# Kernel tuning notes

Hardware: AMD Instinct MI355X
Metric: run time of the kernel (lower is better)

Reference implementation:

```python
import jax, jax.numpy as jnp
import numpy as np

SCALE_FACTOR = 4.0
DROPOUT_P = 0.5
DROPOUT_KEY = jax.random.key(42)  # fixed key: torch dropout is stochastic; we fix RNG for reproducibility


def setup_inputs() -> dict:
    key = jax.random.key(0)
    k1, k2 = jax.random.split(key)
    x1 = jax.random.normal(k1, (4096, 1024), dtype=jnp.float32)
    x2 = jax.random.normal(k2, (4096, 1024), dtype=jnp.float32)
    return {"x1": x1, "x2": x2}


def reference(x1, x2):
    # scores: [M, N] = x1 @ x2^T, scaled
    scores = jnp.matmul(x1, x2.T) * SCALE_FACTOR
    # F.softmax with no dim on 2-D input -> softmax over dim 1 (keys)
    attn = jax.nn.softmax(scores, axis=-1)
    # dropout p=0.5, train mode (inverted dropout: scale kept units by 1/(1-p))
    keep = jax.random.bernoulli(DROPOUT_KEY, 1.0 - DROPOUT_P, attn.shape)
    attn = jnp.where(keep, attn / (1.0 - DROPOUT_P), 0.0).astype(attn.dtype)
    # output: [M, D] = attn @ x2 (x2 reused as values)
    return jnp.matmul(attn, x2)
```

## Files before the change

kernel.cpp:

```cpp
#include <hip/hip_runtime.h>

typedef unsigned short u16;
typedef unsigned int   u32;
typedef __attribute__((ext_vector_type(4))) float f32x4;
typedef __attribute__((ext_vector_type(8))) short bf16x8;
typedef __attribute__((ext_vector_type(8))) unsigned short u16x8;
typedef __attribute__((ext_vector_type(4))) unsigned short u16x4;

#define MROWS 4096
#define DDIM  1024

__device__ __forceinline__ u16 f2bf(float f) {
  u32 u = __float_as_uint(f);
  return (u16)((u + 0x7FFFu + ((u >> 16) & 1u)) >> 16);
}
__device__ __forceinline__ float bf2f(u16 h) { return __uint_as_float(((u32)h) << 16); }

__device__ __forceinline__ u32 rotl32(u32 x, int r) { return (x << r) | (x >> (32 - r)); }
__device__ __forceinline__ u32 threefry_bits(u32 n) {
  const u32 K0 = 0u, K1 = 42u, K2 = 0x1BD11BDAu ^ 0u ^ 42u;
  u32 x0 = K0;
  u32 x1 = n + K1;
#define TF4(a,b,c,d) \
  x0 += x1; x1 = rotl32(x1, a); x1 ^= x0; \
  x0 += x1; x1 = rotl32(x1, b); x1 ^= x0; \
  x0 += x1; x1 = rotl32(x1, c); x1 ^= x0; \
  x0 += x1; x1 = rotl32(x1, d); x1 ^= x0;
  TF4(13,15,26,6);  x0 += K1; x1 += K2 + 1u;
  TF4(17,29,16,24); x0 += K2; x1 += K0 + 2u;
  TF4(13,15,26,6);  x0 += K0; x1 += K1 + 3u;
  TF4(17,29,16,24); x0 += K1; x1 += K2 + 4u;
  TF4(13,15,26,6);  x0 += K2; x1 += K0 + 5u;
#undef TF4
  return x0 ^ x1;
}

__global__ __launch_bounds__(256)
void expand3(const float4* __restrict__ x, u16* __restrict__ out, float scale, int patA,
             u32* __restrict__ mask, u32 wordBase, u32 nWords) {
  int t = blockIdx.x * 256 + threadIdx.x;
  float4 v0 = x[(size_t)t * 2], v1 = x[(size_t)t * 2 + 1];
  float vv[8] = {v0.x*scale, v0.y*scale, v0.z*scale, v0.w*scale,
                 v1.x*scale, v1.y*scale, v1.z*scale, v1.w*scale};
  u16 o[24];
#pragma unroll
  for (int j = 0; j < 8; ++j) {
    u16 h = f2bf(vv[j]);
    u16 l = f2bf(vv[j] - bf2f(h));
    if (patA) { o[3*j]=h; o[3*j+1]=h; o[3*j+2]=l; }
    else      { o[3*j]=h; o[3*j+1]=l; o[3*j+2]=h; }
  }
  u16x8* dst = (u16x8*)(out + (size_t)t * 24);
#pragma unroll
  for (int q = 0; q < 3; ++q) {
    u16x8 wv;
#pragma unroll
    for (int j = 0; j < 8; ++j) wv[j] = o[q*8+j];
    dst[q] = wv;
  }
  if ((u32)t < nWords) {
    u32 wi = wordBase + (u32)t;
    u32 n0 = wi * 32u;
    u32 wbits = 0;
#pragma unroll 4
    for (int b = 0; b < 32; ++b) wbits |= (threefry_bits(n0 + (u32)b) >> 31) << b;
    mask[wi] = wbits;
  }
}

__global__ __launch_bounds__(256)
void transpose_bf16(const float* __restrict__ x2, u16* __restrict__ VT) {
  __shared__ float tile[64][65];
  int tid = threadIdx.x;
  int dt = blockIdx.x;
  int kt = blockIdx.y;
#pragma unroll
  for (int it = 0; it < 16; ++it) {
    int lin = it * 256 + tid;
    int r = lin >> 6, c = lin & 63;
    tile[r][c] = x2[(size_t)(kt*64 + r) * DDIM + dt*64 + c];
  }
  __syncthreads();
#pragma unroll
  for (int it = 0; it < 16; ++it) {
    int lin = it * 256 + tid;
    int dr = lin >> 6, kc = lin & 63;
    VT[(size_t)(dt*64 + dr) * MROWS + kt*64 + kc] = f2bf(tile[kc][dr]);
  }
}

__device__ __forceinline__ void gload16(const u16* g, u16* l) {
  __builtin_amdgcn_global_load_lds(
      (const __attribute__((address_space(1))) void*)g,
      (__attribute__((address_space(3))) void*)l, 16, 0, 0);
}

#define BARRIER() do { asm volatile("" ::: "memory"); __builtin_amdgcn_s_barrier(); \
                       asm volatile("" ::: "memory"); } while (0)
#define LGKM0()   do { asm volatile("s_waitcnt lgkmcnt(0)" ::: "memory"); \
                       __builtin_amdgcn_sched_barrier(0); } while (0)
#define VMCNT6()  do { asm volatile("s_waitcnt vmcnt(6)" ::: "memory"); } while (0)

__device__ __forceinline__ void mma4x4(f32x4 (&accq)[4][4], const bf16x8 (&a)[4],
                                       const bf16x8 (&b)[4]) {
#pragma unroll
  for (int m = 0; m < 4; ++m)
#pragma unroll
    for (int n = 0; n < 4; ++n)
      accq[m][n] = __builtin_amdgcn_mfma_f32_16x16x32_bf16(a[m], b[n], accq[m][n], 0, 0, 0);
}

__global__ __launch_bounds__(512, 2)
void gemm256(const u16* __restrict__ A, const u16* __restrict__ Bt, float* __restrict__ C,
             int M, int N, int K, int ntpc) {
  __shared__ u16 smem[65536];
  const int tid = threadIdx.x;
  const int lane = tid & 63;
  const int w = tid >> 6;
  const int wr = w >> 2;
  const int wc = w & 3;
  const int fr = lane & 15;
  const int hi = lane >> 4;

  const int nbxy = gridDim.x * gridDim.y;
  const int id0 = blockIdx.y * gridDim.x + blockIdx.x;
  const int id  = (id0 & 7) * (nbxy >> 3) + (id0 >> 3);
  const int bxi = id % gridDim.x;
  const int byi = id / gridDim.x;

  const long bm = (long)byi * 256;
  const long bn = (long)bxi * 256;
  const size_t kcol0 = (size_t)blockIdx.z * ntpc * 64;
  float* Cz = C + (size_t)blockIdx.z * (size_t)M * N;

  const int srow = tid >> 3;
  const int scol = (((tid & 7) ^ (srow & 7)) << 3);
  const u16* Abase = A  + (size_t)(bm + srow) * K + kcol0 + scol;
  const u16* Bbase = Bt + (size_t)(bn + srow) * K + kcol0 + scol;

  const int csw0 = ((hi)     ^ (fr & 7)) << 3;
  const int csw1 = ((4 + hi) ^ (fr & 7)) << 3;
  const int arow = (wr*16 + fr) * 64;
  const int brow = (wc*16 + fr) * 64;

#define RD_A(dst, D, H, CSW) do { \
    const u16* _b = smem + ((D)*2+(H))*8192 + arow + (CSW); \
    dst[0] = *(const bf16x8*)(_b); \
    dst[1] = *(const bf16x8*)(_b + 2048); \
    dst[2] = *(const bf16x8*)(_b + 4096); \
    dst[3] = *(const bf16x8*)(_b + 6144); } while (0)
#define RD_B(dst, D, CSW) do { \
    const u16* _b0 = smem + 32768 + ((D)*2+0)*8192 + brow + (CSW); \
    const u16* _b1 = smem + 32768 + ((D)*2+1)*8192 + brow + (CSW); \
    dst[0] = *(const bf16x8*)(_b0); \
    dst[1] = *(const bf16x8*)(_b0 + 4096); \
    dst[2] = *(const bf16x8*)(_b1); \
    dst[3] = *(const bf16x8*)(_b1 + 4096); } while (0)

  f32x4 accL[4][4], accH[4][4];
#pragma unroll
  for (int m = 0; m < 4; ++m)
#pragma unroll
    for (int n = 0; n < 4; ++n) {
      accL[m][n] = (f32x4){0.f, 0.f, 0.f, 0.f};
      accH[m][n] = (f32x4){0.f, 0.f, 0.f, 0.f};
    }
  bf16x8 aE[4], aO[4], bE[4], bO[4];

#define STAGE_A(TAU,H,D) do { \
    const u16* _s = Abase + (size_t)(H)*128*K + (size_t)(TAU)*64; \
    u16* _d = smem + ((D)*2+(H))*8192 + tid*8; \
    gload16(_s, _d); gload16(_s + (size_t)64*K, _d + 4096); } while (0)
#define STAGE_B(TAU,H,D) do { \
    const u16* _s = Bbase + (size_t)(H)*128*K + (size_t)(TAU)*64; \
    u16* _d = smem + 32768 + ((D)*2+(H))*8192 + tid*8; \
    gload16(_s, _d); gload16(_s + (size_t)64*K, _d + 4096); } while (0)

  STAGE_A(0,0,0); STAGE_B(0,0,0); STAGE_B(0,1,0); STAGE_A(0,1,0);
  STAGE_A(1,0,1); STAGE_B(1,0,1); STAGE_B(1,1,1);
  VMCNT6();
  BARRIER();

  const int nt = ntpc;
  for (int T = 0; T < nt; T += 2) {
    const int t1 = T + 1;
    const int t2 = (T + 2 < nt) ? T + 2 : nt - 1;
    const int t3 = (T + 3 < nt) ? T + 3 : nt - 1;

    RD_A(aE, 0, 0, csw0);
    RD_B(bE, 0, csw0);
    STAGE_A(t1, 1, 1);
    BARRIER(); LGKM0();
    __builtin_amdgcn_s_setprio(1); mma4x4(accL, aE, bE); __builtin_amdgcn_s_setprio(0);
    BARRIER();
    RD_A(aO, 0, 0, csw1);
    RD_B(bO, 0, csw1);
    BARRIER(); LGKM0();
    __builtin_amdgcn_s_setprio(1); mma4x4(accL, aO, bO); __builtin_amdgcn_s_setprio(0);
    BARRIER();
    RD_A(aE, 0, 1, csw0);
    STAGE_A(t2, 0, 0); STAGE_B(t2, 0, 0); STAGE_B(t2, 1, 0);
    BARRIER(); LGKM0();
    __builtin_amdgcn_s_setprio(1); mma4x4(accH, aE, bE); __builtin_amdgcn_s_setprio(0);
    BARRIER();
    RD_A(aO, 0, 1, csw1);
    VMCNT6();
    BARRIER(); LGKM0();
    __builtin_amdgcn_s_setprio(1); mma4x4(accH, aO, bO); __builtin_amdgcn_s_setprio(0);
    BARRIER();
    RD_A(aE, 1, 0, csw0);
    RD_B(bE, 1, csw0);
    STAGE_A(t2, 1, 0);
    BARRIER(); LGKM0();
    __builtin_amdgcn_s_setprio(1); mma4x4(accL, aE, bE); __builtin_amdgcn_s_setprio(0);
    BARRIER();
    RD_A(aO, 1, 0, csw1);
    RD_B(bO, 1, csw1);
    BARRIER(); LGKM0();
    __builtin_amdgcn_s_setprio(1); mma4x4(accL, aO, bO); __builtin_amdgcn_s_setprio(0);
    BARRIER();
    RD_A(aE, 1, 1, csw0);
    STAGE_A(t3, 0, 1); STAGE_B(t3, 0, 1); STAGE_B(t3, 1, 1);
    BARRIER(); LGKM0();
    __builtin_amdgcn_s_setprio(1); mma4x4(accH, aE, bE); __builtin_amdgcn_s_setprio(0);
    BARRIER();
    RD_A(aO, 1, 1, csw1);
    VMCNT6();
    BARRIER(); LGKM0();
    __builtin_amdgcn_s_setprio(1); mma4x4(accH, aO, bO); __builtin_amdgcn_s_setprio(0);
    BARRIER();
  }
#undef STAGE_A
#undef STAGE_B
#undef RD_A
#undef RD_B

#pragma unroll
  for (int m = 0; m < 4; ++m)
#pragma unroll
    for (int n = 0; n < 4; ++n) {
      size_t rowL = (size_t)(bm + m*32 + wr*16 + hi*4);
      size_t rowH = rowL + 128;
      size_t col  = (size_t)(bn + n*64 + wc*16 + fr);
#pragma unroll
      for (int r = 0; r < 4; ++r) {
        Cz[(rowL + r) * N + col] = accL[m][n][r];
        Cz[(rowH + r) * N + col] = accH[m][n][r];
      }
    }
}

__global__ __launch_bounds__(256)
void softmax_dropout(const float* __restrict__ S, const u32* __restrict__ mask,
                     u16* __restrict__ P) {
  const int tid  = threadIdx.x;
  const int lane = tid & 63;
  const int w    = tid >> 6;
  const int row  = blockIdx.x * 4 + w;
  const float4* Sr = (const float4*)(S + (size_t)row * MROWS);
  float4 v[16];
#pragma unroll
  for (int i = 0; i < 16; ++i) v[i] = Sr[i * 64 + lane];
  float m = -3.0e38f;
#pragma unroll
  for (int i = 0; i < 16; ++i)
    m = fmaxf(m, fmaxf(fmaxf(v[i].x, v[i].y), fmaxf(v[i].z, v[i].w)));
#pragma unroll
  for (int off = 32; off > 0; off >>= 1) m = fmaxf(m, __shfl_xor(m, off, 64));
  float s = 0.0f;
#pragma unroll
  for (int i = 0; i < 16; ++i) {
    v[i].x = __expf(v[i].x - m); v[i].y = __expf(v[i].y - m);
    v[i].z = __expf(v[i].z - m); v[i].w = __expf(v[i].w - m);
    s += v[i].x + v[i].y + v[i].z + v[i].w;
  }
#pragma unroll
  for (int off = 32; off > 0; off >>= 1) s += __shfl_xor(s, off, 64);
  const float inv = 2.0f / s;
  u16* Pr = P + (size_t)row * MROWS;
  const u32* Mw = mask + (size_t)row * 128;
#pragma unroll
  for (int i = 0; i < 16; ++i) {
    int j0 = (i * 64 + lane) * 4;
    u32 word = Mw[j0 >> 5];
    int sh = j0 & 31;
    float e[4] = {v[i].x, v[i].y, v[i].z, v[i].w};
    u16x4 o;
#pragma unroll
    for (int c = 0; c < 4; ++c) {
      float val = ((word >> (sh + c)) & 1u) ? 0.0f : e[c] * inv;
      o[c] = f2bf(val);
    }
    *(u16x4*)(Pr + j0) = o;
  }
}

__global__ __launch_bounds__(256)
void reduce4(const float4* __restrict__ p, float4* __restrict__ out) {
  size_t i = (size_t)blockIdx.x * 256 + threadIdx.x;
  const size_t NP = (size_t)MROWS * DDIM / 4;
  float4 a = p[i], b = p[i + NP], c = p[i + 2*NP], d = p[i + 3*NP];
  float4 r;
  r.x = a.x + b.x + c.x + d.x;
  r.y = a.y + b.y + c.y + d.y;
  r.z = a.z + b.z + c.z + d.z;
  r.w = a.w + b.w + c.w + d.w;
  out[i] = r;
}

extern "C" void kernel_launch(void* const* d_in, const int* in_sizes, int n_in,
                              void* d_out, int out_size, void* d_ws, size_t ws_size,
                              hipStream_t stream) {
  const float* x1 = (const float*)d_in[0];
  const float* x2 = (const float*)d_in[1];
  float* out = (float*)d_out;
  char* ws = (char*)d_ws;

  const size_t OFF_XB   = 25165824;
  const size_t OFF_VT   = 50331648;
  const size_t OFF_S    = 58720256;
  const size_t OFF_MASK = 125829120;
  const size_t NEED     = 127926272;
  if (ws_size < NEED) {
    hipMemsetAsync(d_out, 0x7F, (size_t)out_size * sizeof(float), stream);
    return;
  }
  u16*   XA = (u16*)(ws);
  u16*   XB = (u16*)(ws + OFF_XB);
  u16*   VT = (u16*)(ws + OFF_VT);
  float* S  = (float*)(ws + OFF_S);
  float* PT = (float*)(ws + OFF_S);
  u32*   MK = (u32*)(ws + OFF_MASK);
  u16*   P  = (u16*)(ws);

  expand3<<<2048, 256, 0, stream>>>((const float4*)x1, XA, 4.0f, 1, MK, 0u, 262144u);
  expand3<<<2048, 256, 0, stream>>>((const float4*)x2, XB, 1.0f, 0, MK, 262144u, 262144u);
  transpose_bf16<<<dim3(16, 64), 256, 0, stream>>>(x2, VT);
  gemm256<<<dim3(16, 16, 1), 512, 0, stream>>>(XA, XB, S, 4096, 4096, 3072, 48);
  softmax_dropout<<<1024, 256, 0, stream>>>(S, MK, P);
  gemm256<<<dim3(4, 16, 4), 512, 0, stream>>>(P, VT, PT, 4096, 1024, 4096, 16);
  reduce4<<<4096, 256, 0, stream>>>((const float4*)PT, (float4*)out);
}
```

Before: 205.5 us.

## Restructure GEMM pipeline into quadrant MFMAs, bf16 split-K partials, split mask RNG

```diff
diff --git a/kernel.cpp b/kernel.cpp
--- a/kernel.cpp
+++ b/kernel.cpp
@@ -37,7 +37,7 @@
 
 __global__ __launch_bounds__(256)
 void expand3(const float4* __restrict__ x, u16* __restrict__ out, float scale, int patA,
-             u32* __restrict__ mask, u32 wordBase, u32 nWords) {
+             u32* __restrict__ mask, u32 wordBase) {
   int t = blockIdx.x * 256 + threadIdx.x;
   float4 v0 = x[(size_t)t * 2], v1 = x[(size_t)t * 2 + 1];
   float vv[8] = {v0.x*scale, v0.y*scale, v0.z*scale, v0.w*scale,
@@ -58,14 +58,14 @@
     for (int j = 0; j < 8; ++j) wv[j] = o[q*8+j];
     dst[q] = wv;
   }
-  if ((u32)t < nWords) {
-    u32 wi = wordBase + (u32)t;
-    u32 n0 = wi * 32u;
-    u32 wbits = 0;
+  u32 w = wordBase + ((u32)t >> 1);
+  u32 sh = ((u32)t & 1u) << 4;
+  u32 n0 = w * 32u + sh;
+  u32 half = 0;
 #pragma unroll 4
-    for (int b = 0; b < 32; ++b) wbits |= (threefry_bits(n0 + (u32)b) >> 31) << b;
-    mask[wi] = wbits;
-  }
+  for (int b = 0; b < 16; ++b) half |= (threefry_bits(n0 + (u32)b) >> 31) << (sh + b);
+  u32 word = half | (u32)__shfl_xor((int)half, 1, 64);
+  if ((t & 1) == 0) mask[w] = word;
 }
 
 __global__ __launch_bounds__(256)
@@ -97,21 +97,25 @@
 
 #define BARRIER() do { asm volatile("" ::: "memory"); __builtin_amdgcn_s_barrier(); \
                        asm volatile("" ::: "memory"); } while (0)
-#define LGKM0()   do { asm volatile("s_waitcnt lgkmcnt(0)" ::: "memory"); \
-                       __builtin_amdgcn_sched_barrier(0); } while (0)
-#define VMCNT6()  do { asm volatile("s_waitcnt vmcnt(6)" ::: "memory"); } while (0)
-
-__device__ __forceinline__ void mma4x4(f32x4 (&accq)[4][4], const bf16x8 (&a)[4],
-                                       const bf16x8 (&b)[4]) {
-#pragma unroll
-  for (int m = 0; m < 4; ++m)
-#pragma unroll
-    for (int n = 0; n < 4; ++n)
-      accq[m][n] = __builtin_amdgcn_mfma_f32_16x16x32_bf16(a[m], b[n], accq[m][n], 0, 0, 0);
-}
-
+#define VMCNT(N)  asm volatile("s_waitcnt vmcnt(" #N ")" ::: "memory")
+#define PRIO1()   __builtin_amdgcn_s_setprio(1)
+#define PRIO0()   __builtin_amdgcn_s_setprio(0)
+
+__device__ __forceinline__ void mma_quad(f32x4 (&acc)[8][4], const bf16x8 (&aF)[4][2],
+                                         const bf16x8 (&bF)[2][2], int MH, int NH) {
+#pragma unroll
+  for (int kx = 0; kx < 2; ++kx)
+#pragma unroll
+    for (int m = 0; m < 4; ++m)
+#pragma unroll
+      for (int n = 0; n < 2; ++n)
+        acc[MH*4+m][NH*2+n] = __builtin_amdgcn_mfma_f32_16x16x32_bf16(
+            aF[m][kx], bF[n][kx], acc[MH*4+m][NH*2+n], 0, 0, 0);
+}
+
+template <bool OUT16>
 __global__ __launch_bounds__(512, 2)
-void gemm256(const u16* __restrict__ A, const u16* __restrict__ Bt, float* __restrict__ C,
+void gemm256(const u16* __restrict__ A, const u16* __restrict__ Bt, void* __restrict__ Cv,
              int M, int N, int K, int ntpc) {
   __shared__ u16 smem[65536];
   const int tid = threadIdx.x;
@@ -122,16 +126,9 @@
   const int fr = lane & 15;
   const int hi = lane >> 4;
 
-  const int nbxy = gridDim.x * gridDim.y;
-  const int id0 = blockIdx.y * gridDim.x + blockIdx.x;
-  const int id  = (id0 & 7) * (nbxy >> 3) + (id0 >> 3);
-  const int bxi = id % gridDim.x;
-  const int byi = id / gridDim.x;
-
-  const long bm = (long)byi * 256;
-  const long bn = (long)bxi * 256;
+  const long bm = (long)blockIdx.y * 256;
+  const long bn = (long)blockIdx.x * 256;
   const size_t kcol0 = (size_t)blockIdx.z * ntpc * 64;
-  float* Cz = C + (size_t)blockIdx.z * (size_t)M * N;
 
   const int srow = tid >> 3;
   const int scol = (((tid & 7) ^ (srow & 7)) << 3);
@@ -143,29 +140,25 @@
   const int arow = (wr*16 + fr) * 64;
   const int brow = (wc*16 + fr) * 64;
 
-#define RD_A(dst, D, H, CSW) do { \
-    const u16* _b = smem + ((D)*2+(H))*8192 + arow + (CSW); \
-    dst[0] = *(const bf16x8*)(_b); \
-    dst[1] = *(const bf16x8*)(_b + 2048); \
-    dst[2] = *(const bf16x8*)(_b + 4096); \
-    dst[3] = *(const bf16x8*)(_b + 6144); } while (0)
-#define RD_B(dst, D, CSW) do { \
-    const u16* _b0 = smem + 32768 + ((D)*2+0)*8192 + brow + (CSW); \
-    const u16* _b1 = smem + 32768 + ((D)*2+1)*8192 + brow + (CSW); \
-    dst[0] = *(const bf16x8*)(_b0); \
-    dst[1] = *(const bf16x8*)(_b0 + 4096); \
-    dst[2] = *(const bf16x8*)(_b1); \
-    dst[3] = *(const bf16x8*)(_b1 + 4096); } while (0)
-
-  f32x4 accL[4][4], accH[4][4];
-#pragma unroll
-  for (int m = 0; m < 4; ++m)
-#pragma unroll
-    for (int n = 0; n < 4; ++n) {
-      accL[m][n] = (f32x4){0.f, 0.f, 0.f, 0.f};
-      accH[m][n] = (f32x4){0.f, 0.f, 0.f, 0.f};
-    }
-  bf16x8 aE[4], aO[4], bE[4], bO[4];
+#define RD_A(dst, D, H) do { \
+    const u16* _b0 = smem + ((D)*2+(H))*8192 + arow + csw0; \
+    const u16* _b1 = smem + ((D)*2+(H))*8192 + arow + csw1; \
+    dst[0][0] = *(const bf16x8*)(_b0);        dst[0][1] = *(const bf16x8*)(_b1); \
+    dst[1][0] = *(const bf16x8*)(_b0 + 2048); dst[1][1] = *(const bf16x8*)(_b1 + 2048); \
+    dst[2][0] = *(const bf16x8*)(_b0 + 4096); dst[2][1] = *(const bf16x8*)(_b1 + 4096); \
+    dst[3][0] = *(const bf16x8*)(_b0 + 6144); dst[3][1] = *(const bf16x8*)(_b1 + 6144); } while (0)
+#define RD_B(dst, D, H) do { \
+    const u16* _b0 = smem + 32768 + ((D)*2+(H))*8192 + brow + csw0; \
+    const u16* _b1 = smem + 32768 + ((D)*2+(H))*8192 + brow + csw1; \
+    dst[0][0] = *(const bf16x8*)(_b0);        dst[0][1] = *(const bf16x8*)(_b1); \
+    dst[1][0] = *(const bf16x8*)(_b0 + 4096); dst[1][1] = *(const bf16x8*)(_b1 + 4096); } while (0)
+
+  f32x4 acc[8][4];
+#pragma unroll
+  for (int m = 0; m < 8; ++m)
+#pragma unroll
+    for (int n = 0; n < 4; ++n) acc[m][n] = (f32x4){0.f, 0.f, 0.f, 0.f};
+  bf16x8 a0[4][2], a1[4][2], b0[2][2], b1[2][2];
 
 #define STAGE_A(TAU,H,D) do { \
     const u16* _s = Abase + (size_t)(H)*128*K + (size_t)(TAU)*64; \
@@ -176,59 +169,49 @@
     u16* _d = smem + 32768 + ((D)*2+(H))*8192 + tid*8; \
     gload16(_s, _d); gload16(_s + (size_t)64*K, _d + 4096); } while (0)
 
-  STAGE_A(0,0,0); STAGE_B(0,0,0); STAGE_B(0,1,0); STAGE_A(0,1,0);
-  STAGE_A(1,0,1); STAGE_B(1,0,1); STAGE_B(1,1,1);
-  VMCNT6();
-  BARRIER();
+  STAGE_A(0,0,0); STAGE_B(0,0,0);
+  VMCNT(0); BARRIER();
+  RD_A(a0, 0, 0); RD_B(b0, 0, 0);
+  STAGE_B(0,1,0);
+  STAGE_A(0,1,0);
+  STAGE_A(1,0,1); STAGE_B(1,0,1);
+  STAGE_B(1,1,1);
+  STAGE_A(1,1,1);
+  VMCNT(10); BARRIER();
 
   const int nt = ntpc;
   for (int T = 0; T < nt; T += 2) {
-    const int t1 = T + 1;
     const int t2 = (T + 2 < nt) ? T + 2 : nt - 1;
     const int t3 = (T + 3 < nt) ? T + 3 : nt - 1;
 
-    RD_A(aE, 0, 0, csw0);
-    RD_B(bE, 0, csw0);
-    STAGE_A(t1, 1, 1);
-    BARRIER(); LGKM0();
-    __builtin_amdgcn_s_setprio(1); mma4x4(accL, aE, bE); __builtin_amdgcn_s_setprio(0);
+    RD_B(b1, 0, 1);
+    PRIO1(); mma_quad(acc, a0, b0, 0, 0); PRIO0();
+    VMCNT(8);  BARRIER();
+    RD_A(a1, 0, 1);
+    STAGE_A(t2, 0, 0); STAGE_B(t2, 0, 0);
+    PRIO1(); mma_quad(acc, a0, b1, 0, 1); PRIO0();
     BARRIER();
-    RD_A(aO, 0, 0, csw1);
-    RD_B(bO, 0, csw1);
-    BARRIER(); LGKM0();
-    __builtin_amdgcn_s_setprio(1); mma4x4(accL, aO, bO); __builtin_amdgcn_s_setprio(0);
+    STAGE_B(t2, 1, 0);
+    PRIO1(); mma_quad(acc, a1, b0, 1, 0); PRIO0();
+    VMCNT(10); BARRIER();
+    RD_A(a0, 1, 0); RD_B(b0, 1, 0);
+    STAGE_A(t2, 1, 0);
+    PRIO1(); mma_quad(acc, a1, b1, 1, 1); PRIO0();
+    VMCNT(10); BARRIER();
+    RD_B(b1, 1, 1);
+    PRIO1(); mma_quad(acc, a0, b0, 0, 0); PRIO0();
+    VMCNT(8);  BARRIER();
+    RD_A(a1, 1, 1);
+    STAGE_A(t3, 0, 1); STAGE_B(t3, 0, 1);
+    PRIO1(); mma_quad(acc, a0, b1, 0, 1); PRIO0();
     BARRIER();
-    RD_A(aE, 0, 1, csw0);
-    STAGE_A(t2, 0, 0); STAGE_B(t2, 0, 0); STAGE_B(t2, 1, 0);
-    BARRIER(); LGKM0();
-    __builtin_amdgcn_s_setprio(1); mma4x4(accH, aE, bE); __builtin_amdgcn_s_setprio(0);
-    BARRIER();
-    RD_A(aO, 0, 1, csw1);
-    VMCNT6();
-    BARRIER(); LGKM0();
-    __builtin_amdgcn_s_setprio(1); mma4x4(accH, aO, bO); __builtin_amdgcn_s_setprio(0);
-    BARRIER();
-    RD_A(aE, 1, 0, csw0);
-    RD_B(bE, 1, csw0);
-    STAGE_A(t2, 1, 0);
-    BARRIER(); LGKM0();
-    __builtin_amdgcn_s_setprio(1); mma4x4(accL, aE, bE); __builtin_amdgcn_s_setprio(0);
-    BARRIER();
-    RD_A(aO, 1, 0, csw1);
-    RD_B(bO, 1, csw1);
-    BARRIER(); LGKM0();
-    __builtin_amdgcn_s_setprio(1); mma4x4(accL, aO, bO); __builtin_amdgcn_s_setprio(0);
-    BARRIER();
-    RD_A(aE, 1, 1, csw0);
-    STAGE_A(t3, 0, 1); STAGE_B(t3, 0, 1); STAGE_B(t3, 1, 1);
-    BARRIER(); LGKM0();
-    __builtin_amdgcn_s_setprio(1); mma4x4(accH, aE, bE); __builtin_amdgcn_s_setprio(0);
-    BARRIER();
-    RD_A(aO, 1, 1, csw1);
-    VMCNT6();
-    BARRIER(); LGKM0();
-    __builtin_amdgcn_s_setprio(1); mma4x4(accH, aO, bO); __builtin_amdgcn_s_setprio(0);
-    BARRIER();
+    STAGE_B(t3, 1, 1);
+    PRIO1(); mma_quad(acc, a1, b0, 1, 0); PRIO0();
+    VMCNT(10); BARRIER();
+    RD_A(a0, 0, 0); RD_B(b0, 0, 0);
+    STAGE_A(t3, 1, 1);
+    PRIO1(); mma_quad(acc, a1, b1, 1, 1); PRIO0();
+    VMCNT(10); BARRIER();
   }
 #undef STAGE_A
 #undef STAGE_B
@@ -236,16 +219,20 @@
 #undef RD_B
 
 #pragma unroll
-  for (int m = 0; m < 4; ++m)
+  for (int m = 0; m < 8; ++m)
 #pragma unroll
     for (int n = 0; n < 4; ++n) {
-      size_t rowL = (size_t)(bm + m*32 + wr*16 + hi*4);
-      size_t rowH = rowL + 128;
+      size_t row0 = (size_t)(bm + m*32 + wr*16 + hi*4);
       size_t col  = (size_t)(bn + n*64 + wc*16 + fr);
 #pragma unroll
       for (int r = 0; r < 4; ++r) {
-        Cz[(rowL + r) * N + col] = accL[m][n][r];
-        Cz[(rowH + r) * N + col] = accH[m][n][r];
+        if (OUT16) {
+          u16* Cz = (u16*)Cv + (size_t)blockIdx.z * (size_t)M * N;
+          Cz[(row0 + r) * N + col] = f2bf(acc[m][n][r]);
+        } else {
+          float* Cz = (float*)Cv + (size_t)blockIdx.z * (size_t)M * N;
+          Cz[(row0 + r) * N + col] = acc[m][n][r];
+        }
       }
     }
 }
@@ -296,15 +283,18 @@
 }
 
 __global__ __launch_bounds__(256)
-void reduce4(const float4* __restrict__ p, float4* __restrict__ out) {
+void reduce4(const u16* __restrict__ p, float4* __restrict__ out) {
   size_t i = (size_t)blockIdx.x * 256 + threadIdx.x;
-  const size_t NP = (size_t)MROWS * DDIM / 4;
-  float4 a = p[i], b = p[i + NP], c = p[i + 2*NP], d = p[i + 3*NP];
+  const size_t NP = (size_t)MROWS * DDIM;
+  u16x4 a = *(const u16x4*)(p + i*4);
+  u16x4 b = *(const u16x4*)(p + NP + i*4);
+  u16x4 c = *(const u16x4*)(p + 2*NP + i*4);
+  u16x4 d = *(const u16x4*)(p + 3*NP + i*4);
   float4 r;
-  r.x = a.x + b.x + c.x + d.x;
-  r.y = a.y + b.y + c.y + d.y;
-  r.z = a.z + b.z + c.z + d.z;
-  r.w = a.w + b.w + c.w + d.w;
+  r.x = bf2f(a[0]) + bf2f(b[0]) + bf2f(c[0]) + bf2f(d[0]);
+  r.y = bf2f(a[1]) + bf2f(b[1]) + bf2f(c[1]) + bf2f(d[1]);
+  r.z = bf2f(a[2]) + bf2f(b[2]) + bf2f(c[2]) + bf2f(d[2]);
+  r.w = bf2f(a[3]) + bf2f(b[3]) + bf2f(c[3]) + bf2f(d[3]);
   out[i] = r;
 }
 
@@ -329,15 +319,15 @@
   u16*   XB = (u16*)(ws + OFF_XB);
   u16*   VT = (u16*)(ws + OFF_VT);
   float* S  = (float*)(ws + OFF_S);
-  float* PT = (float*)(ws + OFF_S);
+  u16*   PT = (u16*)(ws + OFF_S);
   u32*   MK = (u32*)(ws + OFF_MASK);
   u16*   P  = (u16*)(ws);
 
-  expand3<<<2048, 256, 0, stream>>>((const float4*)x1, XA, 4.0f, 1, MK, 0u, 262144u);
-  expand3<<<2048, 256, 0, stream>>>((const float4*)x2, XB, 1.0f, 0, MK, 262144u, 262144u);
+  expand3<<<2048, 256, 0, stream>>>((const float4*)x1, XA, 4.0f, 1, MK, 0u);
+  expand3<<<2048, 256, 0, stream>>>((const float4*)x2, XB, 1.0f, 0, MK, 262144u);
   transpose_bf16<<<dim3(16, 64), 256, 0, stream>>>(x2, VT);
-  gemm256<<<dim3(16, 16, 1), 512, 0, stream>>>(XA, XB, S, 4096, 4096, 3072, 48);
+  gemm256<false><<<dim3(16, 16, 1), 512, 0, stream>>>(XA, XB, S, 4096, 4096, 3072, 48);
   softmax_dropout<<<1024, 256, 0, stream>>>(S, MK, P);
-  gemm256<<<dim3(4, 16, 4), 512, 0, stream>>>(P, VT, PT, 4096, 1024, 4096, 16);
-  reduce4<<<4096, 256, 0, stream>>>((const float4*)PT, (float4*)out);
-}
+  gemm256<true><<<dim3(4, 16, 4), 512, 0, stream>>>(P, VT, PT, 4096, 1024, 4096, 16);
+  reduce4<<<4096, 256, 0, stream>>>(PT, (float4*)out);
+}
```

New measurement: 192.0 us. 1.07x faster.
